# Optimization experiments

Hardware: AMD Instinct MI355X
Metric: run time of the kernel (lower is better)

The kernel has to match this reference:

```python
import jax, jax.numpy as jnp
import numpy as np

E, H = 512, 256  # embed_dim, hidden_dim
B, SQ, SK = 2, 512, 512


def _linear_params(k, fin, fout):
    lim = 1.0 / np.sqrt(fin)
    kw, kb = jax.random.split(k)
    W = jax.random.uniform(kw, (fin, fout), minval=-lim, maxval=lim, dtype=jnp.float32)
    b = jax.random.uniform(kb, (fout,), minval=-lim, maxval=lim, dtype=jnp.float32)
    return W, b


def setup_inputs() -> dict:
    rng = jax.random.key(0)
    ks = jax.random.split(rng, 12)
    query = jax.random.normal(ks[0], (B, SQ, E), dtype=jnp.float32)
    key = jax.random.normal(ks[1], (B, SK, E), dtype=jnp.float32)
    Wqe, bqe = _linear_params(ks[2], E, H)
    Wke, bke = _linear_params(ks[3], E, H)
    W1, b1 = _linear_params(ks[4], 2 * H, H)  # importance_predictor layer 0
    W2, b2 = _linear_params(ks[5], H, H)      # layer 1
    W3, b3 = _linear_params(ks[6], H, H)      # layer 2
    Wf, bf = _linear_params(ks[7], H, 1)      # final importance logit
    Wv1, bv1 = _linear_params(ks[8], 2 * H, H)  # variance_estimator layer 0
    Wv2, bv2 = _linear_params(ks[9], H, 1)      # variance_estimator final
    return {"query": query, "key": key,
            "Wqe": Wqe, "bqe": bqe, "Wke": Wke, "bke": bke,
            "W1": W1, "b1": b1, "W2": W2, "b2": b2, "W3": W3, "b3": b3,
            "Wf": Wf, "bf": bf, "Wv1": Wv1, "bv1": bv1, "Wv2": Wv2, "bv2": bv2}


def reference(query, key, Wqe, bqe, Wke, bke, W1, b1, W2, b2, W3, b3, Wf, bf, Wv1, bv1, Wv2, bv2):
    # Encoders (dropout is identity at eval)
    qf = jax.nn.relu(jnp.einsum('bqe,eh->bqh', query, Wqe) + bqe)  # [B,Sq,H]
    kf = jax.nn.relu(jnp.einsum('bke,eh->bkh', key, Wke) + bke)    # [B,Sk,H]

    # First Linear(2H,H) on cat([q,k]) == q@W1[:H] + k@W1[H:]; broadcast over pairs
    qp = jnp.einsum('bqh,hd->bqd', qf, W1[:H])
    kp = jnp.einsum('bkh,hd->bkd', kf, W1[H:])
    h = jax.nn.relu(qp[:, :, None, :] + kp[:, None, :, :] + b1)  # [B,Sq,Sk,H]
    h = jax.nn.relu(jnp.einsum('bqkh,hd->bqkd', h, W2) + b2)
    h = jax.nn.relu(jnp.einsum('bqkh,hd->bqkd', h, W3) + b3)
    importance_logits = (jnp.einsum('bqkh,ho->bqko', h, Wf) + bf)[..., 0]  # [B,Sq,Sk]

    # Variance head: Linear(2H,H) split the same way, ReLU, Linear, Softplus
    vq = jnp.einsum('bqh,hd->bqd', qf, Wv1[:H])
    vk = jnp.einsum('bkh,hd->bkd', kf, Wv1[H:])
    v = jax.nn.relu(vq[:, :, None, :] + vk[:, None, :, :] + bv1)  # [B,Sq,Sk,H]
    estimated_variance = jax.nn.softplus((jnp.einsum('bqkh,ho->bqko', v, Wv2) + bv2)[..., 0])
    return importance_logits, estimated_variance
```

## Files before the change

kernel.cpp:

```cpp
#include <hip/hip_runtime.h>
#include <hip/hip_bf16.h>
#include <cstdint>
#include <cstddef>
#include <cstring>

#define HDIM 256
#define EDIM 512
#define NB   2
#define NSQ  512
#define NSK  512

typedef _Float16 f16x8 __attribute__((ext_vector_type(8)));
typedef _Float16 h2    __attribute__((ext_vector_type(2)));
typedef __fp16   fp16v2 __attribute__((ext_vector_type(2)));
typedef float    f32x4  __attribute__((ext_vector_type(4)));

#define OFF_W2F  0u
#define OFF_W3F  65536u
#define OFF_WQEF 131072u
#define OFF_WKEF 262144u
#define OFF_WCQ  393216u
#define OFF_WCK  524288u
#define OFF_WV2H 655360u
#define F16_WS_END_BYTES 1312768u

union U8 { f16x8 v; h2 h[4]; };

__device__ __forceinline__ ushort2 f2h2(float x, float y) {
  fp16v2 r = __builtin_amdgcn_cvt_pkrtz(x, y);
  ushort2 u;
  __builtin_memcpy(&u, &r, 4);
  return u;
}
__device__ __forceinline__ float relu_(float x) { return x > 0.f ? x : 0.f; }
__device__ __forceinline__ float softplus_(float x) {
  return fmaxf(x, 0.f) + log1pf(expf(-fabsf(x)));
}

__global__ __launch_bounds__(256) void shuffle_weights(
    const float* __restrict__ Wqe, const float* __restrict__ Wke,
    const float* __restrict__ W1,  const float* __restrict__ Wv1,
    const float* __restrict__ W2,  const float* __restrict__ W3,
    const float* __restrict__ Wv2,
    unsigned short* __restrict__ wsb)
{
  __shared__ float sW[32 * 257];
  const int bx = blockIdx.x;
  const int t = threadIdx.x;
  if (bx == 80) {
    if (t < 64) {
      float a = Wv2[t * 4 + 0], b = Wv2[t * 4 + 1];
      float c = Wv2[t * 4 + 2], d = Wv2[t * 4 + 3];
      ushort2 lo = f2h2(a, b), hi = f2h2(c, d);
      ushort4 o; o.x = lo.x; o.y = lo.y; o.z = hi.x; o.w = hi.y;
      *(ushort4*)&wsb[OFF_WV2H + t * 4] = o;
    }
    return;
  }
  const float* src; unsigned short* dst; int s; int S;
  if      (bx <  8) { src = W2;          dst = wsb + OFF_W2F;           s = bx;      S = 8;  }
  else if (bx < 16) { src = W3;          dst = wsb + OFF_W3F;           s = bx - 8;  S = 8;  }
  else if (bx < 32) { src = Wqe;         dst = wsb + OFF_WQEF;          s = bx - 16; S = 16; }
  else if (bx < 48) { src = Wke;         dst = wsb + OFF_WKEF;          s = bx - 32; S = 16; }
  else if (bx < 56) { src = W1;          dst = wsb + OFF_WCQ;           s = bx - 48; S = 8;  }
  else if (bx < 64) { src = Wv1;         dst = wsb + OFF_WCQ + 65536u;  s = bx - 56; S = 8;  }
  else if (bx < 72) { src = W1 + 65536;  dst = wsb + OFF_WCK;           s = bx - 64; S = 8;  }
  else              { src = Wv1 + 65536; dst = wsb + OFF_WCK + 65536u;  s = bx - 72; S = 8;  }

  const int kbase = s * 32;
  #pragma unroll
  for (int it = 0; it < 8; ++it) {
    const int f4 = it * 256 + t;
    const int row = f4 >> 6, c4 = (f4 & 63) * 4;
    float4 v = *(const float4*)(src + (size_t)(kbase + row) * 256 + c4);
    sW[row * 257 + c4 + 0] = v.x; sW[row * 257 + c4 + 1] = v.y;
    sW[row * 257 + c4 + 2] = v.z; sW[row * 257 + c4 + 3] = v.w;
  }
  __syncthreads();

  const int wave = t >> 6, lane = t & 63;
  const int n_in = lane & 15, k0 = (lane >> 4) * 8;
  for (int tt = wave * 4; tt < wave * 4 + 4; ++tt) {
    const int n = tt * 16 + n_in;
    float x[8];
    #pragma unroll
    for (int j = 0; j < 8; ++j) x[j] = sW[(k0 + j) * 257 + n];
    ushort2 p0 = f2h2(x[0], x[1]), p1 = f2h2(x[2], x[3]);
    ushort2 p2 = f2h2(x[4], x[5]), p3 = f2h2(x[6], x[7]);
    ushort4 lo; lo.x = p0.x; lo.y = p0.y; lo.z = p1.x; lo.w = p1.y;
    ushort4 hi; hi.x = p2.x; hi.y = p2.y; hi.z = p3.x; hi.w = p3.y;
    unsigned short* o = dst + ((size_t)(tt * S + s) * 64 + lane) * 8;
    *(ushort4*)&o[0] = lo; *(ushort4*)&o[4] = hi;
  }
}

__global__ __launch_bounds__(256) void encoder_kernel(
    const float* __restrict__ query, const float* __restrict__ key,
    const float* __restrict__ bqe,   const float* __restrict__ bke,
    const float* __restrict__ b1,    const float* __restrict__ bv1,
    const unsigned short* __restrict__ WqeF, const unsigned short* __restrict__ WkeF,
    const unsigned short* __restrict__ WcqF, const unsigned short* __restrict__ WckF,
    _Float16* __restrict__ Pq, _Float16* __restrict__ Pk)
{
  __shared__ unsigned short sX[16 * 520];
  __shared__ unsigned short sF[16 * 264];
  __shared__ float sBe[256];
  __shared__ float sBc[512];

  const int bx   = blockIdx.x;
  const int side = bx >> 6;
  const int rt   = bx & 63;
  const int t    = threadIdx.x;

  const float* Xsrc = side ? key : query;
  const unsigned short* WeF = side ? WkeF : WqeF;
  const unsigned short* WcF = side ? WckF : WcqF;
  _Float16* P = side ? Pk : Pq;

  {
    const int m = t >> 4, ch = t & 15;
    const float* xr = Xsrc + (size_t)(rt * 16 + m) * EDIM;
    #pragma unroll
    for (int j = 0; j < 4; ++j) {
      const int c = ch * 32 + j * 8;
      float4 v0 = *(const float4*)(xr + c);
      float4 v1 = *(const float4*)(xr + c + 4);
      ushort2 p0 = f2h2(v0.x, v0.y), p1 = f2h2(v0.z, v0.w);
      ushort2 p2 = f2h2(v1.x, v1.y), p3 = f2h2(v1.z, v1.w);
      ushort4 lo; lo.x = p0.x; lo.y = p0.y; lo.z = p1.x; lo.w = p1.y;
      ushort4 hi; hi.x = p2.x; hi.y = p2.y; hi.z = p3.x; hi.w = p3.y;
      *(ushort4*)&sX[m * 520 + c] = lo;
      *(ushort4*)&sX[m * 520 + c + 4] = hi;
    }
    sBe[t]       = side ? bke[t] : bqe[t];
    sBc[t]       = side ? 0.f : b1[t];
    sBc[256 + t] = side ? 0.f : bv1[t];
  }
  __syncthreads();

  const int wave = t >> 6, lane = t & 63;
  const int l15 = lane & 15, q4 = lane >> 4;

  f32x4 acc1[4];
  #pragma unroll
  for (int ft = 0; ft < 4; ++ft) acc1[ft] = (f32x4){0.f, 0.f, 0.f, 0.f};

  for (int s = 0; s < 16; ++s) {
    f16x8 af[4], bfr;
    #pragma unroll
    for (int ft = 0; ft < 4; ++ft) {
      const int tg = wave * 4 + ft;
      af[ft] = *(const f16x8*)(WeF + ((size_t)(tg * 16 + s) * 64 + lane) * 8);
    }
    bfr = *(const f16x8*)&sX[l15 * 520 + s * 32 + q4 * 8];
    #pragma unroll
    for (int ft = 0; ft < 4; ++ft)
      acc1[ft] = __builtin_amdgcn_mfma_f32_16x16x32_f16(af[ft], bfr, acc1[ft], 0, 0, 0);
  }

  #pragma unroll
  for (int ft = 0; ft < 4; ++ft) {
    const int tg = wave * 4 + ft;
    const int n0 = tg * 16 + q4 * 4;
    float4 b4 = *(const float4*)&sBe[n0];
    f32x4 a = acc1[ft];
    ushort2 lo = f2h2(relu_(a[0] + b4.x), relu_(a[1] + b4.y));
    ushort2 hi = f2h2(relu_(a[2] + b4.z), relu_(a[3] + b4.w));
    ushort4 h; h.x = lo.x; h.y = lo.y; h.z = hi.x; h.w = hi.y;
    *(ushort4*)&sF[l15 * 264 + n0] = h;
  }
  __syncthreads();

  f32x4 acc2[8];
  #pragma unroll
  for (int ft = 0; ft < 8; ++ft) acc2[ft] = (f32x4){0.f, 0.f, 0.f, 0.f};

  for (int s = 0; s < 8; ++s) {
    f16x8 af[8], bfr;
    #pragma unroll
    for (int ft = 0; ft < 8; ++ft) {
      const int tg = wave * 8 + ft;
      af[ft] = *(const f16x8*)(WcF + ((size_t)(tg * 8 + s) * 64 + lane) * 8);
    }
    bfr = *(const f16x8*)&sF[l15 * 264 + s * 32 + q4 * 8];
    #pragma unroll
    for (int ft = 0; ft < 8; ++ft)
      acc2[ft] = __builtin_amdgcn_mfma_f32_16x16x32_f16(af[ft], bfr, acc2[ft], 0, 0, 0);
  }

  #pragma unroll
  for (int ft = 0; ft < 8; ++ft) {
    const int tg = wave * 8 + ft;
    const int n0 = tg * 16 + q4 * 4;
    float4 bc = *(const float4*)&sBc[n0];
    const int row = rt * 16 + l15;
    f32x4 a = acc2[ft];
    ushort2 lo = f2h2(a[0] + bc.x, a[1] + bc.y);
    ushort2 hi = f2h2(a[2] + bc.z, a[3] + bc.w);
    ushort4 o; o.x = lo.x; o.y = lo.y; o.z = hi.x; o.w = hi.y;
    *(ushort4*)((unsigned short*)P + (size_t)row * 512 + n0) = o;
  }
}

__global__ __launch_bounds__(512, 4) void pair_kernel(
    const _Float16* __restrict__ Pq, const _Float16* __restrict__ Pk,
    const unsigned short* __restrict__ W2F, const unsigned short* __restrict__ W3F,
    const float* __restrict__ b2, const float* __restrict__ b3,
    const float* __restrict__ Wf, const float* __restrict__ bfp,
    const unsigned short* __restrict__ Wv2H, const float* __restrict__ bv2p,
    float* __restrict__ out)
{
  __shared__ __align__(16) unsigned char smem[36864];
  unsigned short* sXH = (unsigned short*)smem;
  float* sB2  = (float*)(smem + 33792);
  float* sB3  = (float*)(smem + 34816);
  float* sWf  = (float*)(smem + 35840);
  float* sRed = (float*)(smem + 33792);

  const int kt = blockIdx.x, qy = blockIdx.y, bz = blockIdx.z;
  const int t = threadIdx.x;
  const _Float16* qpRow = Pq + (size_t)(bz * NSQ + qy) * 512;

  const int wave = t >> 6, lane = t & 63;
  const int l15 = lane & 15, q4 = lane >> 4;

  const unsigned short* a2base = W2F + ((size_t)(wave * 2) * 8 * 64 + lane) * 8;
  const unsigned short* a3base = W3F + ((size_t)(wave * 2) * 8 * 64 + lane) * 8;

  f16x8 afd[2][2];
  afd[0][0] = *(const f16x8*)(a2base);
  afd[0][1] = *(const f16x8*)(a2base + 8 * 64 * 8);

  {
    const int m   = t >> 3;
    const int sub = t & 7;
    const _Float16* kpRow = Pk + (size_t)(bz * NSK + kt * 64 + m) * 512;
    const f16x8 z8 = {0, 0, 0, 0, 0, 0, 0, 0};
    float vpart = 0.f;
    #pragma unroll
    for (int it = 0; it < 4; ++it) {
      const int c = it * 64 + sub * 8;
      f16x8 q8 = *(const f16x8*)(qpRow + c);
      f16x8 k8 = *(const f16x8*)(kpRow + c);
      f16x8 r  = __builtin_elementwise_max(q8 + k8, z8);
      *(f16x8*)&sXH[m * 264 + c] = r;
      f16x8 a8 = *(const f16x8*)(qpRow + 256 + c);
      f16x8 v8 = *(const f16x8*)(kpRow + 256 + c);
      U8 ar; ar.v = __builtin_elementwise_max(a8 + v8, z8);
      U8 w8; w8.v = *(const f16x8*)((const _Float16*)Wv2H + c);
      vpart = __builtin_amdgcn_fdot2(ar.h[0], w8.h[0], vpart, false);
      vpart = __builtin_amdgcn_fdot2(ar.h[1], w8.h[1], vpart, false);
      vpart = __builtin_amdgcn_fdot2(ar.h[2], w8.h[2], vpart, false);
      vpart = __builtin_amdgcn_fdot2(ar.h[3], w8.h[3], vpart, false);
    }
    vpart += __shfl_xor(vpart, 1, 64);
    vpart += __shfl_xor(vpart, 2, 64);
    vpart += __shfl_xor(vpart, 4, 64);
    if (sub == 0) {
      const size_t o = (size_t)(bz * NSQ + qy) * NSK + kt * 64 + m;
      out[(size_t)NB * NSQ * NSK + o] = softplus_(vpart + bv2p[0]);
    }
    if (t < 256) { sB2[t] = b2[t]; sB3[t] = b3[t]; sWf[t] = Wf[t]; }
  }
  __syncthreads();

  f32x4 acc[2][4];
  #pragma unroll
  for (int ft = 0; ft < 2; ++ft)
    #pragma unroll
    for (int pt = 0; pt < 4; ++pt)
      acc[ft][pt] = (f32x4){0.f, 0.f, 0.f, 0.f};

  #pragma unroll
  for (int s = 0; s < 8; ++s) {
    if (s < 7) {
      afd[(s + 1) & 1][0] = *(const f16x8*)(a2base + (size_t)(s + 1) * 512);
      afd[(s + 1) & 1][1] = *(const f16x8*)(a2base + 8 * 64 * 8 + (size_t)(s + 1) * 512);
    }
    f16x8 bfr[4];
    #pragma unroll
    for (int pt = 0; pt < 4; ++pt)
      bfr[pt] = *(const f16x8*)&sXH[(pt * 16 + l15) * 264 + s * 32 + q4 * 8];
    #pragma unroll
    for (int ft = 0; ft < 2; ++ft)
      #pragma unroll
      for (int pt = 0; pt < 4; ++pt)
        acc[ft][pt] = __builtin_amdgcn_mfma_f32_16x16x32_f16(afd[s & 1][ft], bfr[pt], acc[ft][pt], 0, 0, 0);
  }
  __syncthreads();

  afd[0][0] = *(const f16x8*)(a3base);
  afd[0][1] = *(const f16x8*)(a3base + 8 * 64 * 8);

  #pragma unroll
  for (int ft = 0; ft < 2; ++ft) {
    const int tg = wave * 2 + ft;
    const int n0 = tg * 16 + q4 * 4;
    float4 b4 = *(const float4*)&sB2[n0];
    #pragma unroll
    for (int pt = 0; pt < 4; ++pt) {
      const int mr = pt * 16 + l15;
      f32x4 a = acc[ft][pt];
      ushort2 lo = f2h2(relu_(a[0] + b4.x), relu_(a[1] + b4.y));
      ushort2 hi = f2h2(relu_(a[2] + b4.z), relu_(a[3] + b4.w));
      ushort4 h; h.x = lo.x; h.y = lo.y; h.z = hi.x; h.w = hi.y;
      *(ushort4*)&sXH[mr * 264 + n0] = h;
    }
  }
  __syncthreads();

  f32x4 acc2[2][4];
  #pragma unroll
  for (int ft = 0; ft < 2; ++ft)
    #pragma unroll
    for (int pt = 0; pt < 4; ++pt)
      acc2[ft][pt] = (f32x4){0.f, 0.f, 0.f, 0.f};

  #pragma unroll
  for (int s = 0; s < 8; ++s) {
    if (s < 7) {
      afd[(s + 1) & 1][0] = *(const f16x8*)(a3base + (size_t)(s + 1) * 512);
      afd[(s + 1) & 1][1] = *(const f16x8*)(a3base + 8 * 64 * 8 + (size_t)(s + 1) * 512);
    }
    f16x8 bfr[4];
    #pragma unroll
    for (int pt = 0; pt < 4; ++pt)
      bfr[pt] = *(const f16x8*)&sXH[(pt * 16 + l15) * 264 + s * 32 + q4 * 8];
    #pragma unroll
    for (int ft = 0; ft < 2; ++ft)
      #pragma unroll
      for (int pt = 0; pt < 4; ++pt)
        acc2[ft][pt] = __builtin_amdgcn_mfma_f32_16x16x32_f16(afd[s & 1][ft], bfr[pt], acc2[ft][pt], 0, 0, 0);
  }

  float p[4] = {0.f, 0.f, 0.f, 0.f};
  #pragma unroll
  for (int ft = 0; ft < 2; ++ft) {
    const int tg = wave * 2 + ft;
    const int n0 = tg * 16 + q4 * 4;
    float4 b4 = *(const float4*)&sB3[n0];
    float4 w4 = *(const float4*)&sWf[n0];
    #pragma unroll
    for (int pt = 0; pt < 4; ++pt) {
      f32x4 a = acc2[ft][pt];
      p[pt] += relu_(a[0] + b4.x) * w4.x + relu_(a[1] + b4.y) * w4.y
             + relu_(a[2] + b4.z) * w4.z + relu_(a[3] + b4.w) * w4.w;
    }
  }
  __syncthreads();
  #pragma unroll
  for (int pt = 0; pt < 4; ++pt) {
    float v = p[pt];
    v += __shfl_xor(v, 16, 64);
    v += __shfl_xor(v, 32, 64);
    if (lane < 16) sRed[wave * 64 + pt * 16 + lane] = v;
  }
  __syncthreads();

  if (t < 64) {
    const size_t o = (size_t)(bz * NSQ + qy) * NSK + kt * 64 + t;
    float lg = bfp[0];
    #pragma unroll
    for (int w = 0; w < 8; ++w) lg += sRed[w * 64 + t];
    out[o] = lg;
  }
}

extern "C" void kernel_launch(void* const* d_in, const int* in_sizes, int n_in,
                              void* d_out, int out_size, void* d_ws, size_t ws_size,
                              hipStream_t stream)
{
  (void)in_sizes; (void)n_in; (void)out_size; (void)ws_size;
  const float* query = (const float*)d_in[0];
  const float* key   = (const float*)d_in[1];
  const float* Wqe   = (const float*)d_in[2];
  const float* bqe   = (const float*)d_in[3];
  const float* Wke   = (const float*)d_in[4];
  const float* bke   = (const float*)d_in[5];
  const float* W1    = (const float*)d_in[6];
  const float* b1    = (const float*)d_in[7];
  const float* W2    = (const float*)d_in[8];
  const float* b2    = (const float*)d_in[9];
  const float* W3    = (const float*)d_in[10];
  const float* b3    = (const float*)d_in[11];
  const float* Wf    = (const float*)d_in[12];
  const float* bf    = (const float*)d_in[13];
  const float* Wv1   = (const float*)d_in[14];
  const float* bv1   = (const float*)d_in[15];
  const float* Wv2   = (const float*)d_in[16];
  const float* bv2   = (const float*)d_in[17];

  unsigned short* wsb = (unsigned short*)d_ws;
  _Float16* Pq = (_Float16*)((char*)d_ws + F16_WS_END_BYTES);
  _Float16* Pk = Pq + (size_t)1024 * 512;
  float* out = (float*)d_out;

  shuffle_weights<<<81, 256, 0, stream>>>(Wqe, Wke, W1, Wv1, W2, W3, Wv2, wsb);
  encoder_kernel<<<128, 256, 0, stream>>>(query, key, bqe, bke, b1, bv1,
      wsb + OFF_WQEF, wsb + OFF_WKEF, wsb + OFF_WCQ, wsb + OFF_WCK, Pq, Pk);
  pair_kernel<<<dim3(NSK / 64, NSQ, NB), 512, 0, stream>>>(Pq, Pk,
      wsb + OFF_W2F, wsb + OFF_W3F, b2, b3, Wf, bf, wsb + OFF_WV2H, bv2, out);
}
```

Baseline: 275.1 us.

## Split encoder output columns across blocks and double-buffer weight and LDS fragments

The encoder grid doubles from 128 to 256 blocks. Each block now computes half of the 512 projection columns, which gives more parallelism in a small kernel, at the cost of recomputing the first encoder GEMM in both halves. Weight fragments in both encoder GEMMs are prefetched one k-step ahead in register double buffers, and the first load is issued before the barrier. In the pair kernel, LDS B-fragments are software-pipelined one step ahead, and the variance reduction/store is deferred until after the W3 GEMM so it overlaps with other work, at the cost of higher register pressure.

```diff
diff --git a/kernel.cpp b/kernel.cpp
--- a/kernel.cpp
+++ b/kernel.cpp
@@ -108,8 +108,10 @@
   __shared__ float sBc[512];
 
   const int bx   = blockIdx.x;
-  const int side = bx >> 6;
-  const int rt   = bx & 63;
+  const int side = bx >> 7;
+  const int idx  = bx & 127;
+  const int rt   = idx >> 1;
+  const int nh   = idx & 1;
   const int t    = threadIdx.x;
 
   const float* Xsrc = side ? key : query;
@@ -136,26 +138,33 @@
     sBc[t]       = side ? 0.f : b1[t];
     sBc[256 + t] = side ? 0.f : bv1[t];
   }
-  __syncthreads();
 
   const int wave = t >> 6, lane = t & 63;
   const int l15 = lane & 15, q4 = lane >> 4;
 
+  const unsigned short* aeb = WeF + ((size_t)(wave * 4) * 16 * 64 + lane) * 8;
+  f16x8 afe[2][4];
+  #pragma unroll
+  for (int ft = 0; ft < 4; ++ft)
+    afe[0][ft] = *(const f16x8*)(aeb + ft * 8192);
+
+  __syncthreads();
+
   f32x4 acc1[4];
   #pragma unroll
   for (int ft = 0; ft < 4; ++ft) acc1[ft] = (f32x4){0.f, 0.f, 0.f, 0.f};
 
+  #pragma unroll
   for (int s = 0; s < 16; ++s) {
-    f16x8 af[4], bfr;
-    #pragma unroll
-    for (int ft = 0; ft < 4; ++ft) {
-      const int tg = wave * 4 + ft;
-      af[ft] = *(const f16x8*)(WeF + ((size_t)(tg * 16 + s) * 64 + lane) * 8);
-    }
-    bfr = *(const f16x8*)&sX[l15 * 520 + s * 32 + q4 * 8];
+    if (s < 15) {
+      #pragma unroll
+      for (int ft = 0; ft < 4; ++ft)
+        afe[(s + 1) & 1][ft] = *(const f16x8*)(aeb + ft * 8192 + (size_t)(s + 1) * 512);
+    }
+    f16x8 bfr = *(const f16x8*)&sX[l15 * 520 + s * 32 + q4 * 8];
     #pragma unroll
     for (int ft = 0; ft < 4; ++ft)
-      acc1[ft] = __builtin_amdgcn_mfma_f32_16x16x32_f16(af[ft], bfr, acc1[ft], 0, 0, 0);
+      acc1[ft] = __builtin_amdgcn_mfma_f32_16x16x32_f16(afe[s & 1][ft], bfr, acc1[ft], 0, 0, 0);
   }
 
   #pragma unroll
@@ -171,26 +180,32 @@
   }
   __syncthreads();
 
-  f32x4 acc2[8];
-  #pragma unroll
-  for (int ft = 0; ft < 8; ++ft) acc2[ft] = (f32x4){0.f, 0.f, 0.f, 0.f};
-
+  const unsigned short* acb = WcF + ((size_t)(nh * 16 + wave * 4) * 8 * 64 + lane) * 8;
+  f16x8 afc[2][4];
+  #pragma unroll
+  for (int ft = 0; ft < 4; ++ft)
+    afc[0][ft] = *(const f16x8*)(acb + ft * 4096);
+
+  f32x4 acc2[4];
+  #pragma unroll
+  for (int ft = 0; ft < 4; ++ft) acc2[ft] = (f32x4){0.f, 0.f, 0.f, 0.f};
+
+  #pragma unroll
   for (int s = 0; s < 8; ++s) {
-    f16x8 af[8], bfr;
-    #pragma unroll
-    for (int ft = 0; ft < 8; ++ft) {
-      const int tg = wave * 8 + ft;
-      af[ft] = *(const f16x8*)(WcF + ((size_t)(tg * 8 + s) * 64 + lane) * 8);
-    }
-    bfr = *(const f16x8*)&sF[l15 * 264 + s * 32 + q4 * 8];
-    #pragma unroll
-    for (int ft = 0; ft < 8; ++ft)
-      acc2[ft] = __builtin_amdgcn_mfma_f32_16x16x32_f16(af[ft], bfr, acc2[ft], 0, 0, 0);
-  }
-
-  #pragma unroll
-  for (int ft = 0; ft < 8; ++ft) {
-    const int tg = wave * 8 + ft;
+    if (s < 7) {
+      #pragma unroll
+      for (int ft = 0; ft < 4; ++ft)
+        afc[(s + 1) & 1][ft] = *(const f16x8*)(acb + ft * 4096 + (size_t)(s + 1) * 512);
+    }
+    f16x8 bfr = *(const f16x8*)&sF[l15 * 264 + s * 32 + q4 * 8];
+    #pragma unroll
+    for (int ft = 0; ft < 4; ++ft)
+      acc2[ft] = __builtin_amdgcn_mfma_f32_16x16x32_f16(afc[s & 1][ft], bfr, acc2[ft], 0, 0, 0);
+  }
+
+  #pragma unroll
+  for (int ft = 0; ft < 4; ++ft) {
+    const int tg = nh * 16 + wave * 4 + ft;
     const int n0 = tg * 16 + q4 * 4;
     float4 bc = *(const float4*)&sBc[n0];
     const int row = rt * 16 + l15;
@@ -231,12 +246,12 @@
   afd[0][0] = *(const f16x8*)(a2base);
   afd[0][1] = *(const f16x8*)(a2base + 8 * 64 * 8);
 
+  float vpart = 0.f;
   {
     const int m   = t >> 3;
     const int sub = t & 7;
     const _Float16* kpRow = Pk + (size_t)(bz * NSK + kt * 64 + m) * 512;
     const f16x8 z8 = {0, 0, 0, 0, 0, 0, 0, 0};
-    float vpart = 0.f;
     #pragma unroll
     for (int it = 0; it < 4; ++it) {
       const int c = it * 64 + sub * 8;
@@ -253,13 +268,6 @@
       vpart = __builtin_amdgcn_fdot2(ar.h[2], w8.h[2], vpart, false);
       vpart = __builtin_amdgcn_fdot2(ar.h[3], w8.h[3], vpart, false);
     }
-    vpart += __shfl_xor(vpart, 1, 64);
-    vpart += __shfl_xor(vpart, 2, 64);
-    vpart += __shfl_xor(vpart, 4, 64);
-    if (sub == 0) {
-      const size_t o = (size_t)(bz * NSQ + qy) * NSK + kt * 64 + m;
-      out[(size_t)NB * NSQ * NSK + o] = softplus_(vpart + bv2p[0]);
-    }
     if (t < 256) { sB2[t] = b2[t]; sB3[t] = b3[t]; sWf[t] = Wf[t]; }
   }
   __syncthreads();
@@ -270,22 +278,28 @@
     #pragma unroll
     for (int pt = 0; pt < 4; ++pt)
       acc[ft][pt] = (f32x4){0.f, 0.f, 0.f, 0.f};
+
+  f16x8 bcur[4], bnxt[4];
+  #pragma unroll
+  for (int pt = 0; pt < 4; ++pt)
+    bcur[pt] = *(const f16x8*)&sXH[(pt * 16 + l15) * 264 + q4 * 8];
 
   #pragma unroll
   for (int s = 0; s < 8; ++s) {
     if (s < 7) {
       afd[(s + 1) & 1][0] = *(const f16x8*)(a2base + (size_t)(s + 1) * 512);
       afd[(s + 1) & 1][1] = *(const f16x8*)(a2base + 8 * 64 * 8 + (size_t)(s + 1) * 512);
-    }
-    f16x8 bfr[4];
-    #pragma unroll
-    for (int pt = 0; pt < 4; ++pt)
-      bfr[pt] = *(const f16x8*)&sXH[(pt * 16 + l15) * 264 + s * 32 + q4 * 8];
+      #pragma unroll
+      for (int pt = 0; pt < 4; ++pt)
+        bnxt[pt] = *(const f16x8*)&sXH[(pt * 16 + l15) * 264 + (s + 1) * 32 + q4 * 8];
+    }
     #pragma unroll
     for (int ft = 0; ft < 2; ++ft)
       #pragma unroll
       for (int pt = 0; pt < 4; ++pt)
-        acc[ft][pt] = __builtin_amdgcn_mfma_f32_16x16x32_f16(afd[s & 1][ft], bfr[pt], acc[ft][pt], 0, 0, 0);
+        acc[ft][pt] = __builtin_amdgcn_mfma_f32_16x16x32_f16(afd[s & 1][ft], bcur[pt], acc[ft][pt], 0, 0, 0);
+    #pragma unroll
+    for (int pt = 0; pt < 4; ++pt) bcur[pt] = bnxt[pt];
   }
   __syncthreads();
 
@@ -317,20 +331,37 @@
       acc2[ft][pt] = (f32x4){0.f, 0.f, 0.f, 0.f};
 
   #pragma unroll
+  for (int pt = 0; pt < 4; ++pt)
+    bcur[pt] = *(const f16x8*)&sXH[(pt * 16 + l15) * 264 + q4 * 8];
+
+  #pragma unroll
   for (int s = 0; s < 8; ++s) {
     if (s < 7) {
       afd[(s + 1) & 1][0] = *(const f16x8*)(a3base + (size_t)(s + 1) * 512);
       afd[(s + 1) & 1][1] = *(const f16x8*)(a3base + 8 * 64 * 8 + (size_t)(s + 1) * 512);
-    }
-    f16x8 bfr[4];
-    #pragma unroll
-    for (int pt = 0; pt < 4; ++pt)
-      bfr[pt] = *(const f16x8*)&sXH[(pt * 16 + l15) * 264 + s * 32 + q4 * 8];
+      #pragma unroll
+      for (int pt = 0; pt < 4; ++pt)
+        bnxt[pt] = *(const f16x8*)&sXH[(pt * 16 + l15) * 264 + (s + 1) * 32 + q4 * 8];
+    }
     #pragma unroll
     for (int ft = 0; ft < 2; ++ft)
       #pragma unroll
       for (int pt = 0; pt < 4; ++pt)
-        acc2[ft][pt] = __builtin_amdgcn_mfma_f32_16x16x32_f16(afd[s & 1][ft], bfr[pt], acc2[ft][pt], 0, 0, 0);
+        acc2[ft][pt] = __builtin_amdgcn_mfma_f32_16x16x32_f16(afd[s & 1][ft], bcur[pt], acc2[ft][pt], 0, 0, 0);
+    #pragma unroll
+    for (int pt = 0; pt < 4; ++pt) bcur[pt] = bnxt[pt];
+  }
+
+  {
+    float v = vpart;
+    v += __shfl_xor(v, 1, 64);
+    v += __shfl_xor(v, 2, 64);
+    v += __shfl_xor(v, 4, 64);
+    if ((t & 7) == 0) {
+      const int m = t >> 3;
+      const size_t o = (size_t)(bz * NSQ + qy) * NSK + kt * 64 + m;
+      out[(size_t)NB * NSQ * NSK + o] = softplus_(v + bv2p[0]);
+    }
   }
 
   float p[4] = {0.f, 0.f, 0.f, 0.f};
@@ -396,7 +427,7 @@
   float* out = (float*)d_out;
 
   shuffle_weights<<<81, 256, 0, stream>>>(Wqe, Wke, W1, Wv1, W2, W3, Wv2, wsb);
-  encoder_kernel<<<128, 256, 0, stream>>>(query, key, bqe, bke, b1, bv1,
+  encoder_kernel<<<256, 256, 0, stream>>>(query, key, bqe, bke, b1, bv1,
       wsb + OFF_WQEF, wsb + OFF_WKEF, wsb + OFF_WCQ, wsb + OFF_WCK, Pq, Pk);
   pair_kernel<<<dim3(NSK / 64, NSQ, NB), 512, 0, stream>>>(Pq, Pk,
       wsb + OFF_W2F, wsb + OFF_W3F, b2, b3, Wf, bf, wsb + OFF_WV2H, bv2, out);
```

Result: faster. 257.6 us (-6.4%).
